# Performance work log

Measured on AMD Instinct MI355X. Metric: run time of the kernel, lower is better.

Reference implementation:

```python
import jax, jax.numpy as jnp
import numpy as np

N = 50000      # nodes
E = 800000     # edges
DIM = 64       # dim_h (= input_dim)
H = 4          # heads
D = DIM // H   # per-head dim = 16
EDGE_DIM = 16
L = 5          # conv layers
G = 64         # graphs in batch
FINAL = 1
SCALE = 1.0 / np.sqrt(D)


def setup_inputs() -> dict:
    key = jax.random.key(0)
    ks = jax.random.split(key, 12)
    x = jax.random.normal(ks[0], (N, DIM), jnp.float32)
    edge_index = jax.random.randint(ks[1], (2, E), 0, N, dtype=jnp.int32).astype(jnp.int64)
    edge_attr = jax.random.normal(ks[2], (E, EDGE_DIM), jnp.float32)
    batch = jnp.sort(jax.random.randint(ks[3], (N,), 0, G, dtype=jnp.int32).astype(jnp.int64))
    s = 1.0 / np.sqrt(DIM)
    se = 1.0 / np.sqrt(EDGE_DIM)
    Wq = jax.random.normal(ks[4], (L, DIM, DIM), jnp.float32) * s
    Wk = jax.random.normal(ks[5], (L, DIM, DIM), jnp.float32) * s
    Wv = jax.random.normal(ks[6], (L, DIM, DIM), jnp.float32) * s
    We = jax.random.normal(ks[7], (L, EDGE_DIM, DIM), jnp.float32) * se
    Wskip = jax.random.normal(ks[8], (L, DIM, DIM), jnp.float32) * s
    W1 = jax.random.normal(ks[9], (L * DIM, L * DIM), jnp.float32) * (1.0 / np.sqrt(L * DIM))
    b1 = jnp.zeros((L * DIM,), jnp.float32)
    W2 = jax.random.normal(ks[10], (L * DIM, FINAL), jnp.float32) * (1.0 / np.sqrt(L * DIM))
    b2 = jnp.zeros((FINAL,), jnp.float32)
    return dict(x=x, edge_index=edge_index, edge_attr=edge_attr, batch=batch,
                Wq=Wq, Wk=Wk, Wv=Wv, We=We, Wskip=Wskip, W1=W1, b1=b1, W2=W2, b2=b2)


def _conv(x, Wq, Wk, Wv, We, Wsk, src, dst, edge_attr):
    # Edge-featured multi-head attention conv (EINv1 / TransformerConv-style).
    n = x.shape[0]
    q = (x @ Wq).reshape(n, H, D)[dst]                      # [E,H,D] query from dst node
    e = (edge_attr @ We).reshape(-1, H, D)                  # [E,H,D] edge projection
    k = (x @ Wk).reshape(n, H, D)[src] + e                  # [E,H,D]
    v = (x @ Wv).reshape(n, H, D)[src] + e                  # [E,H,D]
    logits = (q * k).sum(-1) * SCALE                        # [E,H]
    m = jax.ops.segment_max(logits, dst, num_segments=n)    # per-dst-node max
    a = jnp.exp(logits - m[dst])
    s = jax.ops.segment_sum(a, dst, num_segments=n)
    alpha = a / (s[dst] + 1e-16)                            # segment softmax over incoming edges
    agg = jax.ops.segment_sum(alpha[..., None] * v, dst, num_segments=n)  # [N,H,D]
    return agg.reshape(n, H * D) + x @ Wsk                  # root/skip connection


def reference(x, edge_index, edge_attr, batch, Wq, Wk, Wv, We, Wskip, W1, b1, W2, b2):
    src, dst = edge_index[0], edge_index[1]
    counts = jax.ops.segment_sum(jnp.ones((x.shape[0],), x.dtype), batch, num_segments=G)
    denom = jnp.maximum(counts, 1.0)[:, None]
    h = x
    pooled = []
    for l in range(L):  # fixed small layer count
        h = jax.nn.relu(_conv(h, Wq[l], Wk[l], Wv[l], We[l], Wskip[l], src, dst, edge_attr))
        pooled.append(jax.ops.segment_sum(h, batch, num_segments=G) / denom)  # global_mean_pool
    hcat = jnp.concatenate(pooled, axis=1)                  # [G, 5*DIM]
    hid = jax.nn.relu(hcat @ W1 + b1)
    out = hid @ W2 + b2                                     # dropout is identity in eval
    return out.reshape(-1)                                  # flatten -> [G*FINAL]
```

## Files before the change

### kernel.cpp

```cpp
#include <hip/hip_runtime.h>
#include <math.h>

#define NN 50000
#define NE 800000
#define GG 64
#define SCAN_BLK 512
#define SCAN_NB ((NN + SCAN_BLK - 1) / SCAN_BLK)
#define CSR_CAP (NE + 4 * NN)
#define NBLK ((NN + 63) / 64)

typedef unsigned int uint;
typedef unsigned short ushort;
typedef __attribute__((ext_vector_type(8))) short short8v;
typedef __attribute__((ext_vector_type(4))) float f32x4;

__device__ __forceinline__ uint bf16r(float x) {
    uint u = __float_as_uint(x);
    return (u + 0x7fffu + ((u >> 16) & 1u)) >> 16;
}

__device__ __forceinline__ float red8(float x) {
    float t;
    t = __int_as_float(__builtin_amdgcn_update_dpp(0, __float_as_int(x), 0xB1, 0xF, 0xF, 1));
    x += t;
    t = __int_as_float(__builtin_amdgcn_update_dpp(0, __float_as_int(x), 0x4E, 0xF, 0xF, 1));
    x += t;
    t = __int_as_float(__builtin_amdgcn_update_dpp(0, __float_as_int(x), 0x141, 0xF, 0xF, 1));
    x += t;
    return x;
}


__global__ void k_bounds(const int* __restrict__ batch, int* __restrict__ bstart,
                         float* __restrict__ inv) {
    __shared__ int sb[65];
    int t = threadIdx.x;
    if (t <= 64) {
        int lo = 0, hi = NN;
        while (lo < hi) { int mid = (lo + hi) >> 1; if (batch[mid] < t) lo = mid + 1; else hi = mid; }
        sb[t] = lo;
        bstart[t] = lo;
    }
    __syncthreads();
    if (t < 64) inv[t] = 1.0f / fmaxf((float)(sb[t + 1] - sb[t]), 1.0f);
}


__global__ __launch_bounds__(256) void k_degrank(const int* __restrict__ dstv,
                                                 int* __restrict__ deg,
                                                 int* __restrict__ rank) {
    int e = blockIdx.x * 256 + threadIdx.x;
    if (e < NE) rank[e] = atomicAdd(&deg[dstv[e]], 1);
}

__global__ __launch_bounds__(SCAN_BLK) void k_scan1(const int* __restrict__ deg,
                                                    int* __restrict__ locoff,
                                                    int* __restrict__ bsum) {
    __shared__ int sh[SCAN_BLK];
    int tid = threadIdx.x;
    int n = blockIdx.x * SCAN_BLK + tid;
    int v = (n < NN) ? ((deg[n] + 3) & ~3) : 0;
    sh[tid] = v;
    __syncthreads();
    for (int off = 1; off < SCAN_BLK; off <<= 1) {
        int t = (tid >= off) ? sh[tid - off] : 0;
        __syncthreads();
        sh[tid] += t;
        __syncthreads();
    }
    if (n < NN) locoff[n] = sh[tid] - v;
    if (tid == SCAN_BLK - 1) bsum[blockIdx.x] = sh[tid];
}

__global__ void k_scan2(int* __restrict__ bsum) {
    __shared__ int sh[128];
    int t = threadIdx.x;
    int v = (t < SCAN_NB) ? bsum[t] : 0;
    sh[t] = v;
    __syncthreads();
    for (int off = 1; off < 128; off <<= 1) {
        int u = (t >= off) ? sh[t - off] : 0;
        __syncthreads();
        sh[t] += u;
        __syncthreads();
    }
    if (t < SCAN_NB) bsum[t] = sh[t] - v;
}

__global__ __launch_bounds__(256) void k_scan3(const int* __restrict__ locoff,
                                               const int* __restrict__ bsum,
                                               int* __restrict__ off) {
    int n = blockIdx.x * 256 + threadIdx.x;
    if (n < NN) off[n] = locoff[n] + bsum[n >> 9];
}

__global__ __launch_bounds__(256) void k_fill(const int* __restrict__ srcv,
                                              const int* __restrict__ dstv,
                                              const float* __restrict__ eattr,
                                              const int* __restrict__ off,
                                              const int* __restrict__ rank,
                                              int* __restrict__ srcp,
                                              ushort* __restrict__ aperm) {
    int e = blockIdx.x * 256 + threadIdx.x;
    if (e >= NE) return;
    int d = dstv[e];
    int p = off[d] + rank[e];
    srcp[p] = srcv[e] << 8;
    const float4* ea = reinterpret_cast<const float4*>(eattr + (size_t)e * 16);
    float4 a = ea[0], b = ea[1], c = ea[2], d4 = ea[3];
    uint4 u0, u1;
    u0.x = bf16r(a.x) | (bf16r(a.y) << 16);
    u0.y = bf16r(a.z) | (bf16r(a.w) << 16);
    u0.z = bf16r(b.x) | (bf16r(b.y) << 16);
    u0.w = bf16r(b.z) | (bf16r(b.w) << 16);
    u1.x = bf16r(c.x) | (bf16r(c.y) << 16);
    u1.y = bf16r(c.z) | (bf16r(c.w) << 16);
    u1.z = bf16r(d4.x) | (bf16r(d4.y) << 16);
    u1.w = bf16r(d4.z) | (bf16r(d4.w) << 16);
    uint4* ap = reinterpret_cast<uint4*>(aperm + (size_t)p * 16);
    ap[0] = u0;
    ap[1] = u1;
}

__global__ __launch_bounds__(256) void k_M(const float* __restrict__ Wq,
                                           const float* __restrict__ We,
                                           float* __restrict__ M) {
    int t = blockIdx.x * 256 + threadIdx.x;
    if (t >= 5 * 64 * 64) return;
    int l = t >> 12, i = (t >> 6) & 63, c = t & 63;
    int hh = c >> 4, j = c & 15;
    const float* wq = Wq + l * 4096 + i * 64 + hh * 16;
    const float* we = We + l * 1024 + j * 64 + hh * 16;
    float acc = 0.f;
#pragma unroll
    for (int dd = 0; dd < 16; ++dd) acc += wq[dd] * we[dd];
    M[t] = acc;
}


__global__ __launch_bounds__(256) void k_wfrag(const float* __restrict__ Wq,
                                               const float* __restrict__ Wk,
                                               const float* __restrict__ Wv,
                                               const float* __restrict__ Wsk,
                                               const float* __restrict__ Mw,
                                               ushort* __restrict__ Wf) {
    int t = blockIdx.x * 256 + threadIdx.x;
    if (t >= 5 * 20 * 2 * 64) return;
    int l = t / (20 * 2 * 64);
    int rem = t % (20 * 2 * 64);
    int nt = rem >> 7, s = (rem >> 6) & 1, lane = rem & 63;
    int c = nt * 16 + (lane & 15);
    int k0 = s * 32 + 8 * (lane >> 4);
    int msel = c >> 6, cc = c & 63;
    const float* W = (msel == 0) ? Wq + l * 4096 :
                     (msel == 1) ? Wk + l * 4096 :
                     (msel == 2) ? Wv + l * 4096 :
                     (msel == 3) ? Wsk + l * 4096 : Mw + l * 4096;
    const float C2 = 0.36067376022224085f;
    float sc = (msel == 0 || msel == 4) ? C2 : 1.0f;
    ushort o[8];
#pragma unroll
    for (int j = 0; j < 8; ++j) o[j] = (ushort)bf16r(W[(k0 + j) * 64 + cc] * sc);
    uint4* dst = reinterpret_cast<uint4*>(Wf + (size_t)t * 8);
    uint4 u;
    u.x = (uint)o[0] | ((uint)o[1] << 16);
    u.y = (uint)o[2] | ((uint)o[3] << 16);
    u.z = (uint)o[4] | ((uint)o[5] << 16);
    u.w = (uint)o[6] | ((uint)o[7] << 16);
    dst[0] = u;
}


template<bool L0>
__global__ __launch_bounds__(256) void k_projm(const float* __restrict__ x,
                                               const ushort* __restrict__ Hin,
                                               const ushort* __restrict__ Wfl,
                                               uint* __restrict__ QQp,
                                               uint* __restrict__ KVp,
                                               float* __restrict__ Sb) {
    int tid = threadIdx.x, lane = tid & 63, wv = tid >> 6;
    int n0 = blockIdx.x * 64;
    int arow = lane & 15, agrp = lane >> 4;

    short8v A[4][2];
#pragma unroll
    for (int mt = 0; mt < 4; ++mt) {
        int node = n0 + mt * 16 + arow;
        if (node >= NN) node = NN - 1;
#pragma unroll
        for (int s = 0; s < 2; ++s) {
            int k0 = s * 32 + agrp * 8;
            if (L0) {
                const float* hp = x + (size_t)node * 64 + k0;
                float4 u = *reinterpret_cast<const float4*>(hp);
                float4 v = *reinterpret_cast<const float4*>(hp + 4);
                short8v a;
                a[0] = (short)bf16r(u.x); a[1] = (short)bf16r(u.y);
                a[2] = (short)bf16r(u.z); a[3] = (short)bf16r(u.w);
                a[4] = (short)bf16r(v.x); a[5] = (short)bf16r(v.y);
                a[6] = (short)bf16r(v.z); a[7] = (short)bf16r(v.w);
                A[mt][s] = a;
            } else {
                A[mt][s] = *reinterpret_cast<const short8v*>(Hin + (size_t)node * 64 + k0);
            }
        }
    }

    int ch = wv * 16 + arow;
    int rb = agrp * 4;
    f32x4 qh[4], kh[4];
    const f32x4 z = {0.f, 0.f, 0.f, 0.f};

#pragma unroll
    for (int ni = 0; ni < 5; ++ni) {
        int ntl = wv + 4 * ni;
        f32x4 acc[4] = {z, z, z, z};
#pragma unroll
        for (int s = 0; s < 2; ++s) {
            short8v B = *reinterpret_cast<const short8v*>(
                Wfl + (((size_t)ntl * 2 + s) * 64 + lane) * 8);
#pragma unroll
            for (int mt = 0; mt < 4; ++mt)
                acc[mt] = __builtin_amdgcn_mfma_f32_16x16x32_bf16(A[mt][s], B, acc[mt], 0, 0, 0);
        }
        if (ni == 0) {
#pragma unroll
            for (int mt = 0; mt < 4; ++mt) qh[mt] = acc[mt];
        } else if (ni == 1) {
#pragma unroll
            for (int mt = 0; mt < 4; ++mt) kh[mt] = acc[mt];
        } else if (ni == 2) {
#pragma unroll
            for (int mt = 0; mt < 4; ++mt)
#pragma unroll
                for (int r = 0; r < 4; ++r) {
                    int node = n0 + mt * 16 + rb + r;
                    if (node < NN)
                        KVp[(size_t)node * 64 + ch] = (bf16r(kh[mt][r]) << 16) | bf16r(acc[mt][r]);
                }
        } else if (ni == 3) {
#pragma unroll
            for (int mt = 0; mt < 4; ++mt)
#pragma unroll
                for (int r = 0; r < 4; ++r) {
                    int node = n0 + mt * 16 + rb + r;
                    if (node < NN) Sb[(size_t)node * 64 + ch] = acc[mt][r];
                }
        } else {
#pragma unroll
            for (int mt = 0; mt < 4; ++mt)
#pragma unroll
                for (int r = 0; r < 4; ++r) {
                    int node = n0 + mt * 16 + rb + r;
                    if (node < NN)
                        QQp[(size_t)node * 64 + ch] = (bf16r(qh[mt][r]) << 16) | bf16r(acc[mt][r]);
                }
        }
    }
}


__global__ __launch_bounds__(256) void k_attn(const uint* __restrict__ QQp,
                                              const uint* __restrict__ KVp,
                                              const float* __restrict__ Sb,
                                              const float* __restrict__ Wel,
                                              const uint* __restrict__ aperm32,
                                              const int* __restrict__ srcp,
                                              const int* __restrict__ offp,
                                              const int* __restrict__ cnt,
                                              ushort* __restrict__ Hout) {
    __shared__ float we[16 * 64];
    int tid = threadIdx.x;
    for (int i = tid; i < 1024; i += 256) we[i] = Wel[i];
    __syncthreads();

    int lane = tid & 63;
    int n = blockIdx.x * 4 + (tid >> 6);
    if (n >= NN) return;

    int pc = lane & 31;
    int eh = lane >> 5;
    int hd = pc >> 3;

    uint2 qq = *reinterpret_cast<const uint2*>(QQp + n * 64 + 2 * pc);
    float qf0  = __uint_as_float(qq.x & 0xffff0000u);
    float qwf0 = __uint_as_float(qq.x << 16);
    float qf1  = __uint_as_float(qq.y & 0xffff0000u);
    float qwf1 = __uint_as_float(qq.y << 16);

    int dg = cnt[n], pos0 = offp[n];
    int npass = (dg + 1) >> 1;
    int nsb = (npass + 1) >> 1;

    const char* kvb = (const char*)KVp + pc * 8;
    const uint* apb = aperm32 + (size_t)pos0 * 8 + (pc & 7) + eh * 8;

    float s = 0.f, av0 = 0.f, av1 = 0.f, aa0 = 0.f, aa1 = 0.f;

    auto ldidx = [&](int j, int4& s4) {
        s4 = (j < nsb) ? *reinterpret_cast<const int4*>(srcp + pos0 + j * 4)
                       : make_int4(0, 0, 0, 0);
    };
    auto issueSB = [&](int j, const int4& s4, uint2 (&kv)[2], uint (&au)[2]) {
        int sn0 = eh ? s4.y : s4.x;
        int sn1 = eh ? s4.w : s4.z;
        kv[0] = *reinterpret_cast<const uint2*>(kvb + sn0);
        kv[1] = *reinterpret_cast<const uint2*>(kvb + sn1);
        const uint* a = apb + (size_t)j * 32;
        au[0] = a[0];
        au[1] = a[16];
    };
    auto computeSB = [&](int j, const uint2 (&kv)[2], const uint (&au)[2]) {
#pragma unroll
        for (int p = 0; p < 2; ++p) {
            float kf0 = __uint_as_float(kv[p].x & 0xffff0000u);
            float vf0 = __uint_as_float(kv[p].x << 16);
            float kf1 = __uint_as_float(kv[p].y & 0xffff0000u);
            float vf1 = __uint_as_float(kv[p].y << 16);
            float af0 = __uint_as_float(au[p] << 16);
            float af1 = __uint_as_float(au[p] & 0xffff0000u);
            float d = qf0 * kf0;
            d = fmaf(qf1, kf1, d);
            d = fmaf(qwf0, af0, d);
            d = fmaf(qwf1, af1, d);
            d = red8(d);
            int ei = j * 4 + p * 2 + eh;
            float l = (ei < dg) ? d : -1e30f;
            float a = __builtin_amdgcn_exp2f(l);
            s += a;
            av0 = fmaf(a, vf0, av0);
            av1 = fmaf(a, vf1, av1);
            aa0 = fmaf(a, af0, aa0);
            aa1 = fmaf(a, af1, aa1);
        }
    };

    int4 s4a, s4b;
    uint2 kvA[2], kvB[2];
    uint auA[2], auB[2];

    ldidx(0, s4a);
    issueSB(0, s4a, kvA, auA);
    ldidx(1, s4b);

    int sb = 0;
    while (sb + 1 < nsb) {
        issueSB(sb + 1, s4b, kvB, auB);
        ldidx(sb + 2, s4a);
        computeSB(sb, kvA, auA);
        if (sb + 2 < nsb) {
            issueSB(sb + 2, s4a, kvA, auA);
            ldidx(sb + 3, s4b);
        }
        computeSB(sb + 1, kvB, auB);
        sb += 2;
    }
    if (sb < nsb) computeSB(sb, kvA, auA);

    s   += __shfl_xor(s, 32);
    av0 += __shfl_xor(av0, 32);
    av1 += __shfl_xor(av1, 32);
    aa0 += __shfl_xor(aa0, 32);
    aa1 += __shfl_xor(aa1, 32);

    float rden = 1.0f / (s + 1e-16f);
    float e0 = 0.f, e1 = 0.f;
#pragma unroll
    for (int t = 0; t < 8; ++t) {
        float ae = __shfl(aa0, hd * 8 + t, 32);
        float ao = __shfl(aa1, hd * 8 + t, 32);
        float2 wE = *reinterpret_cast<const float2*>(&we[(2 * t) * 64 + 2 * pc]);
        float2 wO = *reinterpret_cast<const float2*>(&we[(2 * t + 1) * 64 + 2 * pc]);
        e0 = fmaf(ae, wE.x, fmaf(ao, wO.x, e0));
        e1 = fmaf(ae, wE.y, fmaf(ao, wO.y, e1));
    }
    float2 sb2 = *reinterpret_cast<const float2*>(Sb + n * 64 + 2 * pc);
    float hn0 = fmaxf(fmaf(av0 + e0, rden, sb2.x), 0.f);
    float hn1 = fmaxf(fmaf(av1 + e1, rden, sb2.y), 0.f);
    if (lane < 32) {
        uint hw = bf16r(hn0) | (bf16r(hn1) << 16);
        reinterpret_cast<uint*>(Hout)[(size_t)n * 32 + pc] = hw;
    }
}


__global__ __launch_bounds__(512) void k_pool5(const ushort* __restrict__ Hb,
                                               const int* __restrict__ bstart,
                                               const float* __restrict__ inv,
                                               float* __restrict__ hcat) {
    __shared__ float red[512];
    int l = blockIdx.x >> 6, g = blockIdx.x & 63;
    int lo = bstart[g], hi = bstart[g + 1];
    const ushort* H = Hb + (size_t)l * NN * 64;
    int ch = threadIdx.x & 63, ro = threadIdx.x >> 6;
    float acc = 0.f;
    for (int r = lo + ro; r < hi; r += 8)
        acc += __uint_as_float((uint)H[(size_t)r * 64 + ch] << 16);
    red[threadIdx.x] = acc;
    __syncthreads();
    if (ro < 4) red[threadIdx.x] += red[threadIdx.x + 256];
    __syncthreads();
    if (ro < 2) red[threadIdx.x] += red[threadIdx.x + 128];
    __syncthreads();
    if (ro == 0)
        hcat[g * 320 + l * 64 + ch] = (red[ch] + red[64 + ch]) * inv[g];
}


__global__ __launch_bounds__(256) void k_mlp(const float* __restrict__ hcat,
                                             const float* __restrict__ W1,
                                             const float* __restrict__ b1,
                                             const float* __restrict__ W2,
                                             const float* __restrict__ b2,
                                             float* __restrict__ out) {
    __shared__ float hc[320];
    __shared__ float red[256];
    int g = blockIdx.x, tid = threadIdx.x;
    for (int i = tid; i < 320; i += 256) hc[i] = hcat[g * 320 + i];
    __syncthreads();
    float part = 0.f;
    for (int j = tid; j < 320; j += 256) {
        float t = b1[j];
        for (int k = 0; k < 320; ++k) t = fmaf(hc[k], W1[k * 320 + j], t);
        part = fmaf(fmaxf(t, 0.f), W2[j], part);
    }
    red[tid] = part;
    __syncthreads();
    for (int off = 128; off > 0; off >>= 1) {
        if (tid < off) red[tid] += red[tid + off];
        __syncthreads();
    }
    if (tid == 0) out[g] = red[0] + b2[0];
}


extern "C" void kernel_launch(void* const* d_in, const int* in_sizes, int n_in,
                              void* d_out, int out_size, void* d_ws, size_t ws_size,
                              hipStream_t stream) {
    const float* x     = (const float*)d_in[0];
    const int*   ei    = (const int*)d_in[1];
    const float* eattr = (const float*)d_in[2];
    const int*   batch = (const int*)d_in[3];
    const float* Wq    = (const float*)d_in[4];
    const float* Wk    = (const float*)d_in[5];
    const float* Wv    = (const float*)d_in[6];
    const float* We    = (const float*)d_in[7];
    const float* Wsk   = (const float*)d_in[8];
    const float* W1    = (const float*)d_in[9];
    const float* b1    = (const float*)d_in[10];
    const float* W2    = (const float*)d_in[11];
    const float* b2    = (const float*)d_in[12];
    float* out = (float*)d_out;

    const int* srcv = ei;
    const int* dstv = ei + NE;

    float* ws = (float*)d_ws;
    size_t o = 0;
    uint*   QQp = (uint*)(ws + o); o += (size_t)NN * 64;
    uint*   KVp = (uint*)(ws + o); o += (size_t)NN * 64;
    float*  Sb  = ws + o;          o += (size_t)NN * 64;
    ushort* Hb  = (ushort*)(ws + o); o += (size_t)5 * NN * 64 / 2;
    float*  Mw  = ws + o;          o += 5 * 4096;
    ushort* Wf  = (ushort*)(ws + o); o += 5 * 20 * 2 * 64 * 8 / 2;
    float*  inv = ws + o;          o += GG;
    float*  hcat = ws + o;         o += GG * 320;
    int*    bstart = (int*)(ws + o); o += 68;
    int*    deg  = (int*)(ws + o); o += NN;
    int*    srcp = (int*)(ws + o); o += CSR_CAP;
    size_t  zwords = (size_t)NN + CSR_CAP;
    int*    rank   = (int*)(ws + o); o += NE;
    int*    off    = (int*)(ws + o); o += NN;
    int*    locoff = (int*)(ws + o); o += NN;
    int*    bsum   = (int*)(ws + o); o += 128;
    ushort* aperm  = (ushort*)(ws + o); o += (size_t)CSR_CAP * 8;

    hipMemsetAsync(deg, 0, zwords * 4, stream);

    k_bounds<<<1, 128, 0, stream>>>(batch, bstart, inv);
    k_degrank<<<(NE + 255) / 256, 256, 0, stream>>>(dstv, deg, rank);
    k_scan1<<<SCAN_NB, SCAN_BLK, 0, stream>>>(deg, locoff, bsum);
    k_scan2<<<1, 128, 0, stream>>>(bsum);
    k_scan3<<<(NN + 255) / 256, 256, 0, stream>>>(locoff, bsum, off);
    k_fill<<<(NE + 255) / 256, 256, 0, stream>>>(srcv, dstv, eattr, off, rank, srcp, aperm);
    k_M<<<(5 * 4096 + 255) / 256, 256, 0, stream>>>(Wq, We, Mw);
    k_wfrag<<<50, 256, 0, stream>>>(Wq, Wk, Wv, Wsk, Mw, Wf);

    for (int l = 0; l < 5; ++l) {
        const ushort* Wfl = Wf + (size_t)l * 20 * 2 * 64 * 8;
        if (l == 0)
            k_projm<true><<<NBLK, 256, 0, stream>>>(x, Hb, Wfl, QQp, KVp, Sb);
        else
            k_projm<false><<<NBLK, 256, 0, stream>>>(x, Hb + (size_t)(l - 1) * NN * 64,
                                                     Wfl, QQp, KVp, Sb);
        k_attn<<<(NN + 3) / 4, 256, 0, stream>>>(QQp, KVp, Sb,
                                                 We + l * 1024,
                                                 (const uint*)aperm,
                                                 srcp, off, deg,
                                                 Hb + (size_t)l * NN * 64);
    }
    k_pool5<<<320, 512, 0, stream>>>(Hb, bstart, inv, hcat);
    k_mlp<<<GG, 256, 0, stream>>>(hcat, W1, b1, W2, b2, out);
}
```

Before: 456.4 us.

## Fuse preprocessing kernels and interleave permuted edge attributes for paired loads

Merges the batch-bounds search into the second scan kernel, drops the separate offset kernel by computing locoff+bsum inline, and folds the Wq·We product into the weight-fragment kernel, cutting several launches. Edge-attribute permutation is split into a coalesced scatter of bf16 attributes plus an edge-to-position map, followed by a gather that writes an interleaved layout. That layout lets the attention kernel fetch both edges' attribute words with one 8-byte load instead of two scalar loads. It costs extra memory traffic in the setup phase (an additional buffer and a larger memset).

```diff
diff --git a/kernel.cpp b/kernel.cpp
--- a/kernel.cpp
+++ b/kernel.cpp
@@ -31,21 +31,6 @@
 }
 
 
-__global__ void k_bounds(const int* __restrict__ batch, int* __restrict__ bstart,
-                         float* __restrict__ inv) {
-    __shared__ int sb[65];
-    int t = threadIdx.x;
-    if (t <= 64) {
-        int lo = 0, hi = NN;
-        while (lo < hi) { int mid = (lo + hi) >> 1; if (batch[mid] < t) lo = mid + 1; else hi = mid; }
-        sb[t] = lo;
-        bstart[t] = lo;
-    }
-    __syncthreads();
-    if (t < 64) inv[t] = 1.0f / fmaxf((float)(sb[t + 1] - sb[t]), 1.0f);
-}
-
-
 __global__ __launch_bounds__(256) void k_degrank(const int* __restrict__ dstv,
                                                  int* __restrict__ deg,
                                                  int* __restrict__ rank) {
@@ -72,8 +57,12 @@
     if (tid == SCAN_BLK - 1) bsum[blockIdx.x] = sh[tid];
 }
 
-__global__ void k_scan2(int* __restrict__ bsum) {
+__global__ void k_scan2b(int* __restrict__ bsum,
+                         const int* __restrict__ batch,
+                         int* __restrict__ bstart,
+                         float* __restrict__ inv) {
     __shared__ int sh[128];
+    __shared__ int sb[65];
     int t = threadIdx.x;
     int v = (t < SCAN_NB) ? bsum[t] : 0;
     sh[t] = v;
@@ -85,27 +74,31 @@
         __syncthreads();
     }
     if (t < SCAN_NB) bsum[t] = sh[t] - v;
-}
-
-__global__ __launch_bounds__(256) void k_scan3(const int* __restrict__ locoff,
-                                               const int* __restrict__ bsum,
-                                               int* __restrict__ off) {
-    int n = blockIdx.x * 256 + threadIdx.x;
-    if (n < NN) off[n] = locoff[n] + bsum[n >> 9];
-}
-
-__global__ __launch_bounds__(256) void k_fill(const int* __restrict__ srcv,
-                                              const int* __restrict__ dstv,
-                                              const float* __restrict__ eattr,
-                                              const int* __restrict__ off,
-                                              const int* __restrict__ rank,
-                                              int* __restrict__ srcp,
-                                              ushort* __restrict__ aperm) {
+    if (t <= 64) {
+        int lo = 0, hi = NN;
+        while (lo < hi) { int mid = (lo + hi) >> 1; if (batch[mid] < t) lo = mid + 1; else hi = mid; }
+        sb[t] = lo;
+        bstart[t] = lo;
+    }
+    __syncthreads();
+    if (t < 64) inv[t] = 1.0f / fmaxf((float)(sb[t + 1] - sb[t]), 1.0f);
+}
+
+__global__ __launch_bounds__(256) void k_scatter(const int* __restrict__ srcv,
+                                                 const int* __restrict__ dstv,
+                                                 const float* __restrict__ eattr,
+                                                 const int* __restrict__ locoff,
+                                                 const int* __restrict__ bsum,
+                                                 const int* __restrict__ rank,
+                                                 int* __restrict__ srcp,
+                                                 int* __restrict__ e2p,
+                                                 uint* __restrict__ ea16) {
     int e = blockIdx.x * 256 + threadIdx.x;
     if (e >= NE) return;
     int d = dstv[e];
-    int p = off[d] + rank[e];
+    int p = locoff[d] + bsum[d >> 9] + rank[e];
     srcp[p] = srcv[e] << 8;
+    e2p[p] = e;
     const float4* ea = reinterpret_cast<const float4*>(eattr + (size_t)e * 16);
     float4 a = ea[0], b = ea[1], c = ea[2], d4 = ea[3];
     uint4 u0, u1;
@@ -117,24 +110,22 @@
     u1.y = bf16r(c.z) | (bf16r(c.w) << 16);
     u1.z = bf16r(d4.x) | (bf16r(d4.y) << 16);
     u1.w = bf16r(d4.z) | (bf16r(d4.w) << 16);
-    uint4* ap = reinterpret_cast<uint4*>(aperm + (size_t)p * 16);
-    ap[0] = u0;
-    ap[1] = u1;
-}
-
-__global__ __launch_bounds__(256) void k_M(const float* __restrict__ Wq,
-                                           const float* __restrict__ We,
-                                           float* __restrict__ M) {
-    int t = blockIdx.x * 256 + threadIdx.x;
-    if (t >= 5 * 64 * 64) return;
-    int l = t >> 12, i = (t >> 6) & 63, c = t & 63;
-    int hh = c >> 4, j = c & 15;
-    const float* wq = Wq + l * 4096 + i * 64 + hh * 16;
-    const float* we = We + l * 1024 + j * 64 + hh * 16;
-    float acc = 0.f;
-#pragma unroll
-    for (int dd = 0; dd < 16; ++dd) acc += wq[dd] * we[dd];
-    M[t] = acc;
+    uint4* dst = reinterpret_cast<uint4*>(ea16 + (size_t)e * 8);
+    dst[0] = u0;
+    dst[1] = u1;
+}
+
+__global__ __launch_bounds__(256) void k_gather(const int* __restrict__ e2p,
+                                                const uint* __restrict__ ea16,
+                                                uint* __restrict__ aperm32) {
+    int p = blockIdx.x * 256 + threadIdx.x;
+    if (p >= CSR_CAP) return;
+    int e = e2p[p];
+    const uint4* src = reinterpret_cast<const uint4*>(ea16 + (size_t)e * 8);
+    uint4 u0 = src[0], u1 = src[1];
+    uint* base = aperm32 + (size_t)(p >> 2) * 32 + (p & 1) * 16 + ((p >> 1) & 1);
+    base[0]  = u0.x;  base[2]  = u0.y;  base[4]  = u0.z;  base[6]  = u0.w;
+    base[8]  = u1.x;  base[10] = u1.y;  base[12] = u1.z;  base[14] = u1.w;
 }
 
 
@@ -142,7 +133,7 @@
                                                const float* __restrict__ Wk,
                                                const float* __restrict__ Wv,
                                                const float* __restrict__ Wsk,
-                                               const float* __restrict__ Mw,
+                                               const float* __restrict__ We,
                                                ushort* __restrict__ Wf) {
     int t = blockIdx.x * 256 + threadIdx.x;
     if (t >= 5 * 20 * 2 * 64) return;
@@ -152,15 +143,27 @@
     int c = nt * 16 + (lane & 15);
     int k0 = s * 32 + 8 * (lane >> 4);
     int msel = c >> 6, cc = c & 63;
-    const float* W = (msel == 0) ? Wq + l * 4096 :
-                     (msel == 1) ? Wk + l * 4096 :
-                     (msel == 2) ? Wv + l * 4096 :
-                     (msel == 3) ? Wsk + l * 4096 : Mw + l * 4096;
     const float C2 = 0.36067376022224085f;
-    float sc = (msel == 0 || msel == 4) ? C2 : 1.0f;
     ushort o[8];
-#pragma unroll
-    for (int j = 0; j < 8; ++j) o[j] = (ushort)bf16r(W[(k0 + j) * 64 + cc] * sc);
+    if (msel == 4) {
+        int hh = cc >> 4, ja = cc & 15;
+        const float* we = We + l * 1024 + ja * 64 + hh * 16;
+#pragma unroll
+        for (int j = 0; j < 8; ++j) {
+            const float* wq = Wq + l * 4096 + (k0 + j) * 64 + hh * 16;
+            float acc = 0.f;
+#pragma unroll
+            for (int dd = 0; dd < 16; ++dd) acc += wq[dd] * we[dd];
+            o[j] = (ushort)bf16r(acc * C2);
+        }
+    } else {
+        const float* W = (msel == 0) ? Wq + l * 4096 :
+                         (msel == 1) ? Wk + l * 4096 :
+                         (msel == 2) ? Wv + l * 4096 : Wsk + l * 4096;
+        float sc = (msel == 0) ? C2 : 1.0f;
+#pragma unroll
+        for (int j = 0; j < 8; ++j) o[j] = (ushort)bf16r(W[(k0 + j) * 64 + cc] * sc);
+    }
     uint4* dst = reinterpret_cast<uint4*>(Wf + (size_t)t * 8);
     uint4 u;
     u.x = (uint)o[0] | ((uint)o[1] << 16);
@@ -266,7 +269,8 @@
                                               const float* __restrict__ Wel,
                                               const uint* __restrict__ aperm32,
                                               const int* __restrict__ srcp,
-                                              const int* __restrict__ offp,
+                                              const int* __restrict__ locoff,
+                                              const int* __restrict__ bsum,
                                               const int* __restrict__ cnt,
                                               ushort* __restrict__ Hout) {
     __shared__ float we[16 * 64];
@@ -288,12 +292,14 @@
     float qf1  = __uint_as_float(qq.y & 0xffff0000u);
     float qwf1 = __uint_as_float(qq.y << 16);
 
-    int dg = cnt[n], pos0 = offp[n];
+    int dg = cnt[n];
+    int pos0 = locoff[n] + bsum[n >> 9];
     int npass = (dg + 1) >> 1;
     int nsb = (npass + 1) >> 1;
 
     const char* kvb = (const char*)KVp + pc * 8;
-    const uint* apb = aperm32 + (size_t)pos0 * 8 + (pc & 7) + eh * 8;
+    const uint2* apb2 = reinterpret_cast<const uint2*>(aperm32 + (size_t)pos0 * 8)
+                        + (pc & 7) + eh * 8;
 
     float s = 0.f, av0 = 0.f, av1 = 0.f, aa0 = 0.f, aa1 = 0.f;
 
@@ -301,24 +307,23 @@
         s4 = (j < nsb) ? *reinterpret_cast<const int4*>(srcp + pos0 + j * 4)
                        : make_int4(0, 0, 0, 0);
     };
-    auto issueSB = [&](int j, const int4& s4, uint2 (&kv)[2], uint (&au)[2]) {
+    auto issueSB = [&](int j, const int4& s4, uint2 (&kv)[2], uint2& au) {
         int sn0 = eh ? s4.y : s4.x;
         int sn1 = eh ? s4.w : s4.z;
         kv[0] = *reinterpret_cast<const uint2*>(kvb + sn0);
         kv[1] = *reinterpret_cast<const uint2*>(kvb + sn1);
-        const uint* a = apb + (size_t)j * 32;
-        au[0] = a[0];
-        au[1] = a[16];
+        au = apb2[(size_t)j * 16];
     };
-    auto computeSB = [&](int j, const uint2 (&kv)[2], const uint (&au)[2]) {
+    auto computeSB = [&](int j, const uint2 (&kv)[2], const uint2& au) {
 #pragma unroll
         for (int p = 0; p < 2; ++p) {
+            uint a_u = p ? au.y : au.x;
             float kf0 = __uint_as_float(kv[p].x & 0xffff0000u);
             float vf0 = __uint_as_float(kv[p].x << 16);
             float kf1 = __uint_as_float(kv[p].y & 0xffff0000u);
             float vf1 = __uint_as_float(kv[p].y << 16);
-            float af0 = __uint_as_float(au[p] << 16);
-            float af1 = __uint_as_float(au[p] & 0xffff0000u);
+            float af0 = __uint_as_float(a_u << 16);
+            float af1 = __uint_as_float(a_u & 0xffff0000u);
             float d = qf0 * kf0;
             d = fmaf(qf1, kf1, d);
             d = fmaf(qwf0, af0, d);
@@ -337,7 +342,7 @@
 
     int4 s4a, s4b;
     uint2 kvA[2], kvB[2];
-    uint auA[2], auB[2];
+    uint2 auA, auB;
 
     ldidx(0, s4a);
     issueSB(0, s4a, kvA, auA);
@@ -461,30 +466,29 @@
     uint*   KVp = (uint*)(ws + o); o += (size_t)NN * 64;
     float*  Sb  = ws + o;          o += (size_t)NN * 64;
     ushort* Hb  = (ushort*)(ws + o); o += (size_t)5 * NN * 64 / 2;
-    float*  Mw  = ws + o;          o += 5 * 4096;
     ushort* Wf  = (ushort*)(ws + o); o += 5 * 20 * 2 * 64 * 8 / 2;
     float*  inv = ws + o;          o += GG;
     float*  hcat = ws + o;         o += GG * 320;
     int*    bstart = (int*)(ws + o); o += 68;
     int*    deg  = (int*)(ws + o); o += NN;
     int*    srcp = (int*)(ws + o); o += CSR_CAP;
-    size_t  zwords = (size_t)NN + CSR_CAP;
+    int*    e2p  = (int*)(ws + o); o += CSR_CAP;
+    size_t  zwords = (size_t)NN + 2 * (size_t)CSR_CAP;
     int*    rank   = (int*)(ws + o); o += NE;
-    int*    off    = (int*)(ws + o); o += NN;
     int*    locoff = (int*)(ws + o); o += NN;
     int*    bsum   = (int*)(ws + o); o += 128;
+    uint*   ea16   = (uint*)(ws + o); o += (size_t)NE * 8;
     ushort* aperm  = (ushort*)(ws + o); o += (size_t)CSR_CAP * 8;
 
     hipMemsetAsync(deg, 0, zwords * 4, stream);
 
-    k_bounds<<<1, 128, 0, stream>>>(batch, bstart, inv);
     k_degrank<<<(NE + 255) / 256, 256, 0, stream>>>(dstv, deg, rank);
     k_scan1<<<SCAN_NB, SCAN_BLK, 0, stream>>>(deg, locoff, bsum);
-    k_scan2<<<1, 128, 0, stream>>>(bsum);
-    k_scan3<<<(NN + 255) / 256, 256, 0, stream>>>(locoff, bsum, off);
-    k_fill<<<(NE + 255) / 256, 256, 0, stream>>>(srcv, dstv, eattr, off, rank, srcp, aperm);
-    k_M<<<(5 * 4096 + 255) / 256, 256, 0, stream>>>(Wq, We, Mw);
-    k_wfrag<<<50, 256, 0, stream>>>(Wq, Wk, Wv, Wsk, Mw, Wf);
+    k_scan2b<<<1, 128, 0, stream>>>(bsum, batch, bstart, inv);
+    k_scatter<<<(NE + 255) / 256, 256, 0, stream>>>(srcv, dstv, eattr, locoff, bsum,
+                                                    rank, srcp, e2p, ea16);
+    k_gather<<<(CSR_CAP + 255) / 256, 256, 0, stream>>>(e2p, ea16, (uint*)aperm);
+    k_wfrag<<<50, 256, 0, stream>>>(Wq, Wk, Wv, Wsk, We, Wf);
 
     for (int l = 0; l < 5; ++l) {
         const ushort* Wfl = Wf + (size_t)l * 20 * 2 * 64 * 8;
@@ -496,7 +500,7 @@
         k_attn<<<(NN + 3) / 4, 256, 0, stream>>>(QQp, KVp, Sb,
                                                  We + l * 1024,
                                                  (const uint*)aperm,
-                                                 srcp, off, deg,
+                                                 srcp, locoff, bsum, deg,
                                                  Hb + (size_t)l * NN * 64);
     }
     k_pool5<<<320, 512, 0, stream>>>(Hb, bstart, inv, hcat);
```

Measured after the change: 487.4 us. 1.07x slower.
